# Optimization experiments

Measured on AMD Instinct MI355X. Metric: run time of the kernel, lower is better.

The kernel has to match this reference:

```python
import jax, jax.numpy as jnp
import numpy as np

TOP_K = 2

def setup_inputs() -> dict:
    key = jax.random.key(0)
    k1, k2 = jax.random.split(key)
    N, D, E = 16384, 2048, 64
    x = jax.random.normal(k1, (N, D), dtype=jnp.float32)
    W = jax.random.normal(k2, (D, E), dtype=jnp.float32) * (1.0 / np.sqrt(D))
    b = jnp.zeros((E,), dtype=jnp.float32)
    return {"x": x, "W": W, "b": b}

def reference(x, W, b):
    # gate linear: [N, D] @ [D, E] + [E]
    logits = jnp.einsum('nd,de->ne', x, W) + b
    gates = jax.nn.softmax(logits, axis=-1)
    topk_vals, topk_idx = jax.lax.top_k(gates, TOP_K)  # [N, k]
    N = gates.shape[0]
    rows = jnp.arange(N)[:, None]  # [N, 1] broadcast over k
    dispatch_mask = jnp.zeros_like(gates).at[rows, topk_idx].set(topk_vals)
    return dispatch_mask, topk_idx
```

## Files before the change

kernel.cpp:

```cpp
#include <hip/hip_runtime.h>
#include <math.h>

#define NROWS 16384
#define DDIM  2048
#define EEXP  64
#define RB    64
#define KC    128
#define NCH   (DDIM / KC)

#define LVL      16384
#define WBUFO(b) ((b) * 49152)

typedef short  bf16x8 __attribute__((ext_vector_type(8)));
typedef float  f32x16 __attribute__((ext_vector_type(16)));

union V4 { uint4 u; bf16x8 s; };

static __device__ __forceinline__ void split3x2(float f0, float f1,
                                                unsigned int &p0, unsigned int &p1,
                                                unsigned int &p2) {
    unsigned int a0 = __float_as_uint(f0), b0 = __float_as_uint(f1);
    unsigned int ah = a0 & 0xffff0000u,   bh = b0 & 0xffff0000u;
    float fa1 = f0 - __uint_as_float(ah);
    float fb1 = f1 - __uint_as_float(bh);
    unsigned int a1 = __float_as_uint(fa1), b1 = __float_as_uint(fb1);
    unsigned int am = a1 & 0xffff0000u,     bm = b1 & 0xffff0000u;
    float fa2 = fa1 - __uint_as_float(am);
    float fb2 = fb1 - __uint_as_float(bm);
    p0 = (a0 >> 16) | bh;
    p1 = (a1 >> 16) | bm;
    p2 = (__float_as_uint(fa2) >> 16) | (__float_as_uint(fb2) & 0xffff0000u);
}

static __device__ __forceinline__ void cvt8(float4 u, float4 v, V4 &q0, V4 &q1, V4 &q2) {
    split3x2(u.x, u.y, q0.u.x, q1.u.x, q2.u.x);
    split3x2(u.z, u.w, q0.u.y, q1.u.y, q2.u.y);
    split3x2(v.x, v.y, q0.u.z, q1.u.z, q2.u.z);
    split3x2(v.z, v.w, q0.u.w, q1.u.w, q2.u.w);
}

#define MM(ACC, A, B) ACC = __builtin_amdgcn_mfma_f32_32x32x16_bf16((A), (B), ACC, 0, 0, 0)

__global__ __launch_bounds__(512, 2)
void router_kernel(const float* __restrict__ x,
                   const float* __restrict__ W,
                   const float* __restrict__ bias_v,
                   float* __restrict__ mask_out,
                   float* __restrict__ idx_out) {
    __shared__ __align__(16) unsigned char smem[98304];

    const int tid  = threadIdx.x;
    const int lane = tid & 63;
    const int w    = __builtin_amdgcn_readfirstlane(tid >> 6);
    const int row0 = blockIdx.x * RB;
    const int l31  = lane & 31;
    const int h    = lane >> 5;

    const float* xp0 = x + (size_t)(row0 + l31) * DDIM + (w * 16 + h * 8);
    const float* xp1 = xp0 + (size_t)32 * DDIM;

    const int eW = lane;
    const float* wq0 = W + (size_t)(w * 8) * EEXP + eW;
    const float* wq1 = W + (size_t)((w + 8) * 8) * EEXP + eW;
    const int wb0 = eW * 256 + ((w * 16)       ^ ((eW & 7) << 4));
    const int wb1 = eW * 256 + (((w + 8) * 16) ^ ((eW & 7) << 4));

    const int koff = w * 32 + h * 16;
    const int be0  = l31 * 256        + (koff ^ ((l31 & 7) << 4));
    const int be1  = (l31 + 32) * 256 + (koff ^ ((l31 & 7) << 4));

    f32x16 acc0, acc1, acc2, acc3;
#pragma unroll
    for (int i = 0; i < 16; ++i) { acc0[i] = 0.f; acc1[i] = 0.f; acc2[i] = 0.f; acc3[i] = 0.f; }

    float wr0[8], wr1[8];
#pragma unroll
    for (int j = 0; j < 8; ++j) {
        wr0[j] = wq0[(size_t)j * EEXP];
        wr1[j] = wq1[(size_t)j * EEXP];
    }
    {
        unsigned char* d = smem + WBUFO(0);
        V4 q0, q1, q2;
        cvt8(make_float4(wr0[0],wr0[1],wr0[2],wr0[3]),
             make_float4(wr0[4],wr0[5],wr0[6],wr0[7]), q0, q1, q2);
        *(uint4*)(d + wb0) = q0.u; *(uint4*)(d + LVL + wb0) = q1.u; *(uint4*)(d + 2*LVL + wb0) = q2.u;
        cvt8(make_float4(wr1[0],wr1[1],wr1[2],wr1[3]),
             make_float4(wr1[4],wr1[5],wr1[6],wr1[7]), q0, q1, q2);
        *(uint4*)(d + wb1) = q0.u; *(uint4*)(d + LVL + wb1) = q1.u; *(uint4*)(d + 2*LVL + wb1) = q2.u;
    }
    float4 xa00 = *(const float4*)(xp0);
    float4 xa01 = *(const float4*)(xp0 + 4);
    float4 xa10 = *(const float4*)(xp1);
    float4 xa11 = *(const float4*)(xp1 + 4);
    __syncthreads();

#pragma unroll 1
    for (int c = 0; c < NCH; ++c) {
        const int  buf  = c & 1;
        const bool more = (c + 1) < NCH;

        if (more) {
            const float* q0p = wq0 + (size_t)(c + 1) * KC * EEXP;
            const float* q1p = wq1 + (size_t)(c + 1) * KC * EEXP;
#pragma unroll
            for (int j = 0; j < 8; ++j) { wr0[j] = q0p[(size_t)j * EEXP]; wr1[j] = q1p[(size_t)j * EEXP]; }
        }

        V4 a00, a10, a20, a01, a11, a21;
        cvt8(xa00, xa01, a00, a10, a20);
        cvt8(xa10, xa11, a01, a11, a21);

        if (more) {
            xa00 = *(const float4*)(xp0 + (c + 1) * KC);
            xa01 = *(const float4*)(xp0 + (c + 1) * KC + 4);
            xa10 = *(const float4*)(xp1 + (c + 1) * KC);
            xa11 = *(const float4*)(xp1 + (c + 1) * KC + 4);
        }

        const unsigned char* wB = smem + WBUFO(buf);
        bf16x8 b00 = *(const bf16x8*)(wB + be0);
        bf16x8 b01 = *(const bf16x8*)(wB + be1);
        bf16x8 b10 = *(const bf16x8*)(wB + LVL + be0);
        bf16x8 b11 = *(const bf16x8*)(wB + LVL + be1);
        bf16x8 b20 = *(const bf16x8*)(wB + 2 * LVL + be0);
        bf16x8 b21 = *(const bf16x8*)(wB + 2 * LVL + be1);

        MM(acc0, a00.s, b00); MM(acc1, a00.s, b01); MM(acc2, a01.s, b00); MM(acc3, a01.s, b01);
        MM(acc0, a00.s, b10); MM(acc1, a00.s, b11); MM(acc2, a01.s, b10); MM(acc3, a01.s, b11);
        MM(acc0, a10.s, b00); MM(acc1, a10.s, b01); MM(acc2, a11.s, b00); MM(acc3, a11.s, b01);
        MM(acc0, a00.s, b20); MM(acc1, a00.s, b21); MM(acc2, a01.s, b20); MM(acc3, a01.s, b21);
        MM(acc0, a10.s, b10); MM(acc1, a10.s, b11); MM(acc2, a11.s, b10); MM(acc3, a11.s, b11);
        MM(acc0, a20.s, b00); MM(acc1, a20.s, b01); MM(acc2, a21.s, b00); MM(acc3, a21.s, b01);

        if (more) {
            unsigned char* d = smem + WBUFO(buf ^ 1);
            V4 q0, q1, q2;
            cvt8(make_float4(wr0[0],wr0[1],wr0[2],wr0[3]),
                 make_float4(wr0[4],wr0[5],wr0[6],wr0[7]), q0, q1, q2);
            *(uint4*)(d + wb0) = q0.u; *(uint4*)(d + LVL + wb0) = q1.u; *(uint4*)(d + 2*LVL + wb0) = q2.u;
            cvt8(make_float4(wr1[0],wr1[1],wr1[2],wr1[3]),
                 make_float4(wr1[4],wr1[5],wr1[6],wr1[7]), q0, q1, q2);
            *(uint4*)(d + wb1) = q0.u; *(uint4*)(d + LVL + wb1) = q1.u; *(uint4*)(d + 2*LVL + wb1) = q2.u;
        }
        __syncthreads();
    }

    const float bias = bias_v[lane];
    float* ep = (float*)smem;
#pragma unroll
    for (int ph = 0; ph < 2; ++ph) {
        __syncthreads();
#pragma unroll
        for (int r = 0; r < 16; ++r) {
            const int rowl = (r & 3) + 8 * (r >> 2) + 4 * h;
            const float va = (ph == 0) ? acc0[r] : acc2[r];
            const float vb = (ph == 0) ? acc1[r] : acc3[r];
            ep[w * 2048 + rowl * 64 + l31]      = va;
            ep[w * 2048 + rowl * 64 + l31 + 32] = vb;
        }
        __syncthreads();
#pragma unroll
        for (int rr = 0; rr < 4; ++rr) {
            const int rl  = w * 4 + rr;
            const int row = row0 + ph * 32 + rl;
            float logit = bias;
#pragma unroll
            for (int p = 0; p < 8; ++p) logit += ep[p * 2048 + rl * 64 + lane];

            float m = logit;
#pragma unroll
            for (int off = 32; off >= 1; off >>= 1) m = fmaxf(m, __shfl_xor(m, off));
            float ex = __expf(logit - m);
            float s = ex;
#pragma unroll
            for (int off = 32; off >= 1; off >>= 1) s += __shfl_xor(s, off);
            float gate = ex / s;

            float v1 = logit; int i1 = lane;
#pragma unroll
            for (int off = 32; off >= 1; off >>= 1) {
                float ov = __shfl_xor(v1, off);
                int   oi = __shfl_xor(i1, off);
                if (ov > v1 || (ov == v1 && oi < i1)) { v1 = ov; i1 = oi; }
            }
            float v2 = (lane == i1) ? -INFINITY : logit; int i2 = lane;
#pragma unroll
            for (int off = 32; off >= 1; off >>= 1) {
                float ov = __shfl_xor(v2, off);
                int   oi = __shfl_xor(i2, off);
                if (ov > v2 || (ov == v2 && oi < i2)) { v2 = ov; i2 = oi; }
            }

            float outv = (lane == i1 || lane == i2) ? gate : 0.0f;
            mask_out[(size_t)row * EEXP + lane] = outv;
            if (lane == 0) {
                idx_out[row * 2 + 0] = (float)i1;
                idx_out[row * 2 + 1] = (float)i2;
            }
        }
    }
}

extern "C" void kernel_launch(void* const* d_in, const int* in_sizes, int n_in,
                              void* d_out, int out_size, void* d_ws, size_t ws_size,
                              hipStream_t stream) {
    const float* x = (const float*)d_in[0];
    const float* W = (const float*)d_in[1];
    const float* b = (const float*)d_in[2];
    float* mask_out = (float*)d_out;
    float* idx_out  = mask_out + (size_t)NROWS * EEXP;

    dim3 grid(NROWS / RB);
    dim3 block(512);
    router_kernel<<<grid, block, 0, stream>>>(x, W, b, mask_out, idx_out);
}
```

Measured before the change: 219.9 us.

## Halve row block and K chunk, split waves across K groups and expert halves

Shrinks the per-block tile from 64 rows to 32 rows and the K chunk from 128 to 64. The 8 waves are remapped so that four K groups each cover two expert halves, giving one accumulator per wave instead of four. LDS use is halved and the launch bound is raised to 4 blocks per CU, which doubles the grid and is meant to improve occupancy and latency hiding. In exchange, each W chunk is reused across fewer rows, the loop runs twice as many barrier-synchronised iterations, and each wave issues fewer MFMAs per load.

```diff
diff --git a/kernel.cpp b/kernel.cpp
--- a/kernel.cpp
+++ b/kernel.cpp
@@ -4,12 +4,12 @@
 #define NROWS 16384
 #define DDIM  2048
 #define EEXP  64
-#define RB    64
-#define KC    128
+#define RB    32
+#define KC    64
 #define NCH   (DDIM / KC)
 
-#define LVL      16384
-#define WBUFO(b) ((b) * 49152)
+#define LVL     8192
+#define WBUF(b) ((b) * 24576)
 
 typedef short  bf16x8 __attribute__((ext_vector_type(8)));
 typedef float  f32x16 __attribute__((ext_vector_type(16)));
@@ -41,58 +41,49 @@
 
 #define MM(ACC, A, B) ACC = __builtin_amdgcn_mfma_f32_32x32x16_bf16((A), (B), ACC, 0, 0, 0)
 
-__global__ __launch_bounds__(512, 2)
+__global__ __launch_bounds__(512, 4)
 void router_kernel(const float* __restrict__ x,
                    const float* __restrict__ W,
                    const float* __restrict__ bias_v,
                    float* __restrict__ mask_out,
                    float* __restrict__ idx_out) {
-    __shared__ __align__(16) unsigned char smem[98304];
+    __shared__ __align__(16) unsigned char smem[49152];
 
     const int tid  = threadIdx.x;
     const int lane = tid & 63;
     const int w    = __builtin_amdgcn_readfirstlane(tid >> 6);
+    const int kg   = w & 3;
+    const int et   = w >> 2;
     const int row0 = blockIdx.x * RB;
     const int l31  = lane & 31;
     const int h    = lane >> 5;
 
-    const float* xp0 = x + (size_t)(row0 + l31) * DDIM + (w * 16 + h * 8);
-    const float* xp1 = xp0 + (size_t)32 * DDIM;
+    const float* xp = x + (size_t)(row0 + l31) * DDIM + kg * 16 + h * 8;
 
-    const int eW = lane;
-    const float* wq0 = W + (size_t)(w * 8) * EEXP + eW;
-    const float* wq1 = W + (size_t)((w + 8) * 8) * EEXP + eW;
-    const int wb0 = eW * 256 + ((w * 16)       ^ ((eW & 7) << 4));
-    const int wb1 = eW * 256 + (((w + 8) * 16) ^ ((eW & 7) << 4));
+    const float* wq = W + (size_t)(w * 8) * EEXP + lane;
+    const int wb = lane * 128 + ((w * 16) ^ ((lane & 7) << 4));
 
-    const int koff = w * 32 + h * 16;
-    const int be0  = l31 * 256        + (koff ^ ((l31 & 7) << 4));
-    const int be1  = (l31 + 32) * 256 + (koff ^ ((l31 & 7) << 4));
+    const int rB = et * 32 + l31;
+    const int be = rB * 128 + (((2 * kg + h) * 16) ^ ((rB & 7) << 4));
 
-    f32x16 acc0, acc1, acc2, acc3;
+    f32x16 acc;
 #pragma unroll
-    for (int i = 0; i < 16; ++i) { acc0[i] = 0.f; acc1[i] = 0.f; acc2[i] = 0.f; acc3[i] = 0.f; }
+    for (int i = 0; i < 16; ++i) acc[i] = 0.f;
 
-    float wr0[8], wr1[8];
+    float wr[8];
 #pragma unroll
-    for (int j = 0; j < 8; ++j) {
-        wr0[j] = wq0[(size_t)j * EEXP];
-        wr1[j] = wq1[(size_t)j * EEXP];
+    for (int j = 0; j < 8; ++j) wr[j] = wq[(size_t)j * EEXP];
+    {
+        V4 q0, q1, q2;
+        cvt8(make_float4(wr[0], wr[1], wr[2], wr[3]),
+             make_float4(wr[4], wr[5], wr[6], wr[7]), q0, q1, q2);
+        unsigned char* d = smem + WBUF(0);
+        *(uint4*)(d + wb) = q0.u;
+        *(uint4*)(d + LVL + wb) = q1.u;
+        *(uint4*)(d + 2 * LVL + wb) = q2.u;
     }
-    {
-        unsigned char* d = smem + WBUFO(0);
-        V4 q0, q1, q2;
-        cvt8(make_float4(wr0[0],wr0[1],wr0[2],wr0[3]),
-             make_float4(wr0[4],wr0[5],wr0[6],wr0[7]), q0, q1, q2);
-        *(uint4*)(d + wb0) = q0.u; *(uint4*)(d + LVL + wb0) = q1.u; *(uint4*)(d + 2*LVL + wb0) = q2.u;
-        cvt8(make_float4(wr1[0],wr1[1],wr1[2],wr1[3]),
-             make_float4(wr1[4],wr1[5],wr1[6],wr1[7]), q0, q1, q2);
-        *(uint4*)(d + wb1) = q0.u; *(uint4*)(d + LVL + wb1) = q1.u; *(uint4*)(d + 2*LVL + wb1) = q2.u;
-    }
-    float4 xa00 = *(const float4*)(xp0);
-    float4 xa01 = *(const float4*)(xp0 + 4);
-    float4 xa10 = *(const float4*)(xp1);
-    float4 xa11 = *(const float4*)(xp1 + 4);
+    float4 xlo = *(const float4*)(xp);
+    float4 xhi = *(const float4*)(xp + 4);
     __syncthreads();
 
 #pragma unroll 1
@@ -101,47 +92,39 @@
         const bool more = (c + 1) < NCH;
 
         if (more) {
-            const float* q0p = wq0 + (size_t)(c + 1) * KC * EEXP;
-            const float* q1p = wq1 + (size_t)(c + 1) * KC * EEXP;
+            const float* q = wq + (size_t)(c + 1) * KC * EEXP;
 #pragma unroll
-            for (int j = 0; j < 8; ++j) { wr0[j] = q0p[(size_t)j * EEXP]; wr1[j] = q1p[(size_t)j * EEXP]; }
+            for (int j = 0; j < 8; ++j) wr[j] = q[(size_t)j * EEXP];
         }
 
-        V4 a00, a10, a20, a01, a11, a21;
-        cvt8(xa00, xa01, a00, a10, a20);
-        cvt8(xa10, xa11, a01, a11, a21);
+        V4 a0, a1, a2;
+        cvt8(xlo, xhi, a0, a1, a2);
 
         if (more) {
-            xa00 = *(const float4*)(xp0 + (c + 1) * KC);
-            xa01 = *(const float4*)(xp0 + (c + 1) * KC + 4);
-            xa10 = *(const float4*)(xp1 + (c + 1) * KC);
-            xa11 = *(const float4*)(xp1 + (c + 1) * KC + 4);
+            xlo = *(const float4*)(xp + (c + 1) * KC);
+            xhi = *(const float4*)(xp + (c + 1) * KC + 4);
         }
 
-        const unsigned char* wB = smem + WBUFO(buf);
-        bf16x8 b00 = *(const bf16x8*)(wB + be0);
-        bf16x8 b01 = *(const bf16x8*)(wB + be1);
-        bf16x8 b10 = *(const bf16x8*)(wB + LVL + be0);
-        bf16x8 b11 = *(const bf16x8*)(wB + LVL + be1);
-        bf16x8 b20 = *(const bf16x8*)(wB + 2 * LVL + be0);
-        bf16x8 b21 = *(const bf16x8*)(wB + 2 * LVL + be1);
+        const unsigned char* wB = smem + WBUF(buf);
+        bf16x8 b0 = *(const bf16x8*)(wB + be);
+        bf16x8 b1 = *(const bf16x8*)(wB + LVL + be);
+        bf16x8 b2 = *(const bf16x8*)(wB + 2 * LVL + be);
 
-        MM(acc0, a00.s, b00); MM(acc1, a00.s, b01); MM(acc2, a01.s, b00); MM(acc3, a01.s, b01);
-        MM(acc0, a00.s, b10); MM(acc1, a00.s, b11); MM(acc2, a01.s, b10); MM(acc3, a01.s, b11);
-        MM(acc0, a10.s, b00); MM(acc1, a10.s, b01); MM(acc2, a11.s, b00); MM(acc3, a11.s, b01);
-        MM(acc0, a00.s, b20); MM(acc1, a00.s, b21); MM(acc2, a01.s, b20); MM(acc3, a01.s, b21);
-        MM(acc0, a10.s, b10); MM(acc1, a10.s, b11); MM(acc2, a11.s, b10); MM(acc3, a11.s, b11);
-        MM(acc0, a20.s, b00); MM(acc1, a20.s, b01); MM(acc2, a21.s, b00); MM(acc3, a21.s, b01);
+        MM(acc, a0.s, b0);
+        MM(acc, a0.s, b1);
+        MM(acc, a1.s, b0);
+        MM(acc, a0.s, b2);
+        MM(acc, a1.s, b1);
+        MM(acc, a2.s, b0);
 
         if (more) {
-            unsigned char* d = smem + WBUFO(buf ^ 1);
             V4 q0, q1, q2;
-            cvt8(make_float4(wr0[0],wr0[1],wr0[2],wr0[3]),
-                 make_float4(wr0[4],wr0[5],wr0[6],wr0[7]), q0, q1, q2);
-            *(uint4*)(d + wb0) = q0.u; *(uint4*)(d + LVL + wb0) = q1.u; *(uint4*)(d + 2*LVL + wb0) = q2.u;
-            cvt8(make_float4(wr1[0],wr1[1],wr1[2],wr1[3]),
-                 make_float4(wr1[4],wr1[5],wr1[6],wr1[7]), q0, q1, q2);
-            *(uint4*)(d + wb1) = q0.u; *(uint4*)(d + LVL + wb1) = q1.u; *(uint4*)(d + 2*LVL + wb1) = q2.u;
+            cvt8(make_float4(wr[0], wr[1], wr[2], wr[3]),
+                 make_float4(wr[4], wr[5], wr[6], wr[7]), q0, q1, q2);
+            unsigned char* d = smem + WBUF(buf ^ 1);
+            *(uint4*)(d + wb) = q0.u;
+            *(uint4*)(d + LVL + wb) = q1.u;
+            *(uint4*)(d + 2 * LVL + wb) = q2.u;
         }
         __syncthreads();
     }
@@ -149,55 +132,50 @@
     const float bias = bias_v[lane];
     float* ep = (float*)smem;
 #pragma unroll
-    for (int ph = 0; ph < 2; ++ph) {
-        __syncthreads();
+    for (int r = 0; r < 16; ++r) {
+        const int rowl = (r & 3) + 8 * (r >> 2) + 4 * h;
+        ep[kg * 2048 + rowl * 64 + et * 32 + l31] = acc[r];
+    }
+    __syncthreads();
+
 #pragma unroll
-        for (int r = 0; r < 16; ++r) {
-            const int rowl = (r & 3) + 8 * (r >> 2) + 4 * h;
-            const float va = (ph == 0) ? acc0[r] : acc2[r];
-            const float vb = (ph == 0) ? acc1[r] : acc3[r];
-            ep[w * 2048 + rowl * 64 + l31]      = va;
-            ep[w * 2048 + rowl * 64 + l31 + 32] = vb;
+    for (int rr = 0; rr < 4; ++rr) {
+        const int rl  = w * 4 + rr;
+        const int row = row0 + rl;
+        float logit = bias + ep[rl * 64 + lane]
+                           + ep[2048 + rl * 64 + lane]
+                           + ep[4096 + rl * 64 + lane]
+                           + ep[6144 + rl * 64 + lane];
+
+        float m = logit;
+#pragma unroll
+        for (int off = 32; off >= 1; off >>= 1) m = fmaxf(m, __shfl_xor(m, off));
+        float ex = __expf(logit - m);
+        float s = ex;
+#pragma unroll
+        for (int off = 32; off >= 1; off >>= 1) s += __shfl_xor(s, off);
+        float gate = ex / s;
+
+        float v1 = logit; int i1 = lane;
+#pragma unroll
+        for (int off = 32; off >= 1; off >>= 1) {
+            float ov = __shfl_xor(v1, off);
+            int   oi = __shfl_xor(i1, off);
+            if (ov > v1 || (ov == v1 && oi < i1)) { v1 = ov; i1 = oi; }
         }
-        __syncthreads();
+        float v2 = (lane == i1) ? -INFINITY : logit; int i2 = lane;
 #pragma unroll
-        for (int rr = 0; rr < 4; ++rr) {
-            const int rl  = w * 4 + rr;
-            const int row = row0 + ph * 32 + rl;
-            float logit = bias;
-#pragma unroll
-            for (int p = 0; p < 8; ++p) logit += ep[p * 2048 + rl * 64 + lane];
+        for (int off = 32; off >= 1; off >>= 1) {
+            float ov = __shfl_xor(v2, off);
+            int   oi = __shfl_xor(i2, off);
+            if (ov > v2 || (ov == v2 && oi < i2)) { v2 = ov; i2 = oi; }
+        }
 
-            float m = logit;
-#pragma unroll
-            for (int off = 32; off >= 1; off >>= 1) m = fmaxf(m, __shfl_xor(m, off));
-            float ex = __expf(logit - m);
-            float s = ex;
-#pragma unroll
-            for (int off = 32; off >= 1; off >>= 1) s += __shfl_xor(s, off);
-            float gate = ex / s;
-
-            float v1 = logit; int i1 = lane;
-#pragma unroll
-            for (int off = 32; off >= 1; off >>= 1) {
-                float ov = __shfl_xor(v1, off);
-                int   oi = __shfl_xor(i1, off);
-                if (ov > v1 || (ov == v1 && oi < i1)) { v1 = ov; i1 = oi; }
-            }
-            float v2 = (lane == i1) ? -INFINITY : logit; int i2 = lane;
-#pragma unroll
-            for (int off = 32; off >= 1; off >>= 1) {
-                float ov = __shfl_xor(v2, off);
-                int   oi = __shfl_xor(i2, off);
-                if (ov > v2 || (ov == v2 && oi < i2)) { v2 = ov; i2 = oi; }
-            }
-
-            float outv = (lane == i1 || lane == i2) ? gate : 0.0f;
-            mask_out[(size_t)row * EEXP + lane] = outv;
-            if (lane == 0) {
-                idx_out[row * 2 + 0] = (float)i1;
-                idx_out[row * 2 + 1] = (float)i2;
-            }
+        float outv = (lane == i1 || lane == i2) ? gate : 0.0f;
+        mask_out[(size_t)row * EEXP + lane] = outv;
+        if (lane == 0) {
+            idx_out[row * 2 + 0] = (float)i1;
+            idx_out[row * 2 + 1] = (float)i2;
         }
     }
 }
```

Result: no change. 218.0 us (-0.8%).
